# Kernel tuning notes

Measured on AMD Instinct MI355X. Metric: run time of the kernel, lower is better.

The kernel has to match this reference:

```python
import jax, jax.numpy as jnp
import numpy as np

N = 33554432
LABEL = 5
PENALIZE_WEIGHT = 3.0
LOWER = LABEL - 0.5
UPPER = LABEL + 0.5


def setup_inputs() -> dict:
    key = jax.random.key(0)
    k1, k2 = jax.random.split(key)
    x = jax.random.normal(k1, (N,), dtype=jnp.float32)
    t = jax.random.randint(k2, (N,), 0, 10, dtype=jnp.int64)
    return {"input": x, "target": t}


def reference(input, target):
    # Fused elementwise mask: weight = penalize_weight where
    # lower < x < upper AND target != label, else 1.0
    x = input
    penal = (x > LOWER) & (x < UPPER) & (target != LABEL)
    w = jnp.where(penal, jnp.float32(PENALIZE_WEIGHT), jnp.float32(1.0))
    diff = x - target.astype(jnp.float32)
    return jnp.mean(w * diff * diff)
```

## Files before the change

### kernel.cpp

```cpp
#include <hip/hip_runtime.h>


#define LABEL_I   5
#define LOWER_F   4.5f
#define UPPER_F   5.5f
#define PENALTY_F 3.0f

typedef float vf4 __attribute__((ext_vector_type(4)));
typedef int   vi4 __attribute__((ext_vector_type(4)));

__device__ __forceinline__ float term(float x, int t) {
    float d = x - (float)t;
    float w = (x > LOWER_F && x < UPPER_F && t != LABEL_I) ? PENALTY_F : 1.0f;
    return w * d * d;
}

__device__ __forceinline__ float term4(vf4 xv, vi4 tv) {
    return term(xv.x, tv.x) + term(xv.y, tv.y) + term(xv.z, tv.z) + term(xv.w, tv.w);
}

#define TPB 1024

__global__ __launch_bounds__(256, 6) void penal_mse_stage1(
        const vf4* __restrict__ x4,
        const vi4* __restrict__ t4,
        float* __restrict__ partials,
        int n4, int tiles, int n_tail_start, int n_total,
        const float* __restrict__ x_scalar,
        const int*  __restrict__ t_scalar) {
    float s0 = 0.0f, s1 = 0.0f, s2 = 0.0f, s3 = 0.0f;

    for (int tile = blockIdx.x; tile < tiles; tile += gridDim.x) {
        int base = tile * TPB + threadIdx.x;
        const vf4* xp = x4 + base;
        const vi4* tp = t4 + base;
        vf4 a0 = __builtin_nontemporal_load(xp);
        vi4 b0 = __builtin_nontemporal_load(tp);
        vf4 a1 = __builtin_nontemporal_load(xp + 256);
        vi4 b1 = __builtin_nontemporal_load(tp + 256);
        vf4 a2 = __builtin_nontemporal_load(xp + 512);
        vi4 b2 = __builtin_nontemporal_load(tp + 512);
        vf4 a3 = __builtin_nontemporal_load(xp + 768);
        vi4 b3 = __builtin_nontemporal_load(tp + 768);
        asm volatile("" : "+v"(a0), "+v"(b0), "+v"(a1), "+v"(b1),
                          "+v"(a2), "+v"(b2), "+v"(a3), "+v"(b3));
        s0 += term4(a0, b0);
        s1 += term4(a1, b1);
        s2 += term4(a2, b2);
        s3 += term4(a3, b3);
    }

    float sum = (s0 + s1) + (s2 + s3);

    for (int i = tiles * TPB + blockIdx.x * blockDim.x + threadIdx.x;
         i < n4; i += gridDim.x * blockDim.x)
        sum += term4(x4[i], t4[i]);

    for (int j = n_tail_start + blockIdx.x * blockDim.x + threadIdx.x;
         j < n_total; j += gridDim.x * blockDim.x)
        sum += term(x_scalar[j], t_scalar[j]);

    #pragma unroll
    for (int off = 32; off > 0; off >>= 1)
        sum += __shfl_down(sum, off, 64);

    __shared__ float wsum[4];
    int lane = threadIdx.x & 63;
    int wave = threadIdx.x >> 6;
    if (lane == 0) wsum[wave] = sum;
    __syncthreads();

    if (threadIdx.x == 0)
        partials[blockIdx.x] = (wsum[0] + wsum[1]) + (wsum[2] + wsum[3]);
}

__global__ __launch_bounds__(256) void penal_mse_stage2(
        const float* __restrict__ partials, int nparts,
        float* __restrict__ out, float inv_n) {
    float sum = 0.0f;
    for (int i = threadIdx.x; i < nparts; i += 256)
        sum += partials[i];

    #pragma unroll
    for (int off = 32; off > 0; off >>= 1)
        sum += __shfl_down(sum, off, 64);

    __shared__ float wsum[4];
    int lane = threadIdx.x & 63;
    int wave = threadIdx.x >> 6;
    if (lane == 0) wsum[wave] = sum;
    __syncthreads();

    if (threadIdx.x == 0)
        out[0] = ((wsum[0] + wsum[1]) + (wsum[2] + wsum[3])) * inv_n;
}

extern "C" void kernel_launch(void* const* d_in, const int* in_sizes, int n_in,
                              void* d_out, int out_size, void* d_ws, size_t ws_size,
                              hipStream_t stream) {
    const float* x = (const float*)d_in[0];
    const int*   t = (const int*)d_in[1];
    float* out = (float*)d_out;
    float* partials = (float*)d_ws;

    int n  = in_sizes[0];
    int n4 = n >> 2;
    int n_tail_start = n4 << 2;
    int tiles = n4 / TPB;
    float inv_n = 1.0f / (float)n;

    const int block = 256;
    const int grid = 2048;

    penal_mse_stage1<<<grid, block, 0, stream>>>(
        (const vf4*)x, (const vi4*)t, partials,
        n4, tiles, n_tail_start, n, x, t);

    penal_mse_stage2<<<1, block, 0, stream>>>(partials, grid, out, inv_n);
}
```

Before: 252.3 us.

## Software-pipeline loads with double-buffered registers in reduction kernel

```diff
diff --git a/kernel.cpp b/kernel.cpp
--- a/kernel.cpp
+++ b/kernel.cpp
@@ -2,63 +2,90 @@
 
 
 #define LABEL_I   5
-#define LOWER_F   4.5f
-#define UPPER_F   5.5f
+#define LABEL_F   5.0f
 #define PENALTY_F 3.0f
 
 typedef float vf4 __attribute__((ext_vector_type(4)));
 typedef int   vi4 __attribute__((ext_vector_type(4)));
 
-__device__ __forceinline__ float term(float x, int t) {
-    float d = x - (float)t;
-    float w = (x > LOWER_F && x < UPPER_F && t != LABEL_I) ? PENALTY_F : 1.0f;
-    return w * d * d;
+#define TPB  256
+#define GRID 2048
+#define HTV  512
+
+__device__ __forceinline__ void accum4(vf4 xv, vi4 tv, float& acc) {
+#pragma unroll
+    for (int k = 0; k < 4; ++k) {
+        float x = xv[k];
+        int   t = tv[k];
+        float d = x - (float)t;
+        float c = x - LABEL_F;
+        float w = ((__builtin_fabsf(c) < 0.5f) && (t != LABEL_I))
+                      ? PENALTY_F : 1.0f;
+        acc += w * d * d;
+    }
 }
 
-__device__ __forceinline__ float term4(vf4 xv, vi4 tv) {
-    return term(xv.x, tv.x) + term(xv.y, tv.y) + term(xv.z, tv.z) + term(xv.w, tv.w);
-}
-
-#define TPB 1024
-
-__global__ __launch_bounds__(256, 6) void penal_mse_stage1(
+__global__ __launch_bounds__(TPB, 8) void penal_mse_stage1(
         const vf4* __restrict__ x4,
         const vi4* __restrict__ t4,
         float* __restrict__ partials,
-        int n4, int tiles, int n_tail_start, int n_total,
+        int n4, int nht_total, int n_tail_start, int n_total,
         const float* __restrict__ x_scalar,
         const int*  __restrict__ t_scalar) {
-    float s0 = 0.0f, s1 = 0.0f, s2 = 0.0f, s3 = 0.0f;
+    const int tid = threadIdx.x;
+    const int bid = blockIdx.x;
 
-    for (int tile = blockIdx.x; tile < tiles; tile += gridDim.x) {
-        int base = tile * TPB + threadIdx.x;
-        const vf4* xp = x4 + base;
-        const vi4* tp = t4 + base;
-        vf4 a0 = __builtin_nontemporal_load(xp);
-        vi4 b0 = __builtin_nontemporal_load(tp);
-        vf4 a1 = __builtin_nontemporal_load(xp + 256);
-        vi4 b1 = __builtin_nontemporal_load(tp + 256);
-        vf4 a2 = __builtin_nontemporal_load(xp + 512);
-        vi4 b2 = __builtin_nontemporal_load(tp + 512);
-        vf4 a3 = __builtin_nontemporal_load(xp + 768);
-        vi4 b3 = __builtin_nontemporal_load(tp + 768);
-        asm volatile("" : "+v"(a0), "+v"(b0), "+v"(a1), "+v"(b1),
-                          "+v"(a2), "+v"(b2), "+v"(a3), "+v"(b3));
-        s0 += term4(a0, b0);
-        s1 += term4(a1, b1);
-        s2 += term4(a2, b2);
-        s3 += term4(a3, b3);
+    float acc0 = 0.0f, acc1 = 0.0f;
+
+    const int nht = (bid < nht_total) ? ((nht_total - bid + GRID - 1) / GRID) : 0;
+
+    vf4 xa0, xa1, xb0, xb1;
+    vi4 ta0, ta1, tb0, tb1;
+
+    #define HT_BASE(s) (((size_t)bid + (size_t)(s) * GRID) * HTV + (size_t)tid)
+
+    #define LOAD_A(s) do { size_t _o = HT_BASE(s);                         \
+        xa0 = x4[_o]; ta0 = t4[_o]; xa1 = x4[_o + TPB]; ta1 = t4[_o + TPB];\
+        __builtin_amdgcn_sched_barrier(0); } while (0)
+    #define LOAD_B(s) do { size_t _o = HT_BASE(s);                         \
+        xb0 = x4[_o]; tb0 = t4[_o]; xb1 = x4[_o + TPB]; tb1 = t4[_o + TPB];\
+        __builtin_amdgcn_sched_barrier(0); } while (0)
+
+    #define CONSUME_A() do { accum4(xa0, ta0, acc0); accum4(xa1, ta1, acc1); } while (0)
+    #define CONSUME_B() do { accum4(xb0, tb0, acc0); accum4(xb1, tb1, acc1); } while (0)
+
+    int s = 0;
+    if (nht > 0) LOAD_A(0);
+    for (; s + 2 < nht; s += 2) {
+        LOAD_B(s + 1);
+        CONSUME_A();
+        LOAD_A(s + 2);
+        CONSUME_B();
+    }
+    if (nht > 0) {
+        if (nht - s == 2) {
+            LOAD_B(s + 1);
+            CONSUME_A();
+            CONSUME_B();
+        } else {
+            CONSUME_A();
+        }
+    }
+    float sum = acc0 + acc1;
+
+    for (int i = nht_total * HTV + bid * TPB + tid; i < n4; i += GRID * TPB) {
+        vf4 xv = x4[i]; vi4 tv = t4[i];
+        accum4(xv, tv, sum);
     }
 
-    float sum = (s0 + s1) + (s2 + s3);
-
-    for (int i = tiles * TPB + blockIdx.x * blockDim.x + threadIdx.x;
-         i < n4; i += gridDim.x * blockDim.x)
-        sum += term4(x4[i], t4[i]);
-
-    for (int j = n_tail_start + blockIdx.x * blockDim.x + threadIdx.x;
-         j < n_total; j += gridDim.x * blockDim.x)
-        sum += term(x_scalar[j], t_scalar[j]);
+    for (int j = n_tail_start + bid * TPB + tid; j < n_total; j += GRID * TPB) {
+        float x = x_scalar[j];
+        int   t = t_scalar[j];
+        float d = x - (float)t;
+        float c = x - LABEL_F;
+        float w = ((__builtin_fabsf(c) < 0.5f) && (t != LABEL_I)) ? PENALTY_F : 1.0f;
+        sum += w * d * d;
+    }
 
     #pragma unroll
     for (int off = 32; off > 0; off >>= 1)
@@ -105,16 +132,13 @@
 
     int n  = in_sizes[0];
     int n4 = n >> 2;
+    int nht_total = n4 / HTV;
     int n_tail_start = n4 << 2;
-    int tiles = n4 / TPB;
     float inv_n = 1.0f / (float)n;
 
-    const int block = 256;
-    const int grid = 2048;
+    penal_mse_stage1<<<GRID, TPB, 0, stream>>>(
+        (const vf4*)x, (const vi4*)t, partials,
+        n4, nht_total, n_tail_start, n, x, t);
 
-    penal_mse_stage1<<<grid, block, 0, stream>>>(
-        (const vf4*)x, (const vi4*)t, partials,
-        n4, tiles, n_tail_start, n, x, t);
-
-    penal_mse_stage2<<<1, block, 0, stream>>>(partials, grid, out, inv_n);
+    penal_mse_stage2<<<1, TPB, 0, stream>>>(partials, GRID, out, inv_n);
 }
```

New measurement: 275.9 us. +9.3%, slower.
